# Kernel tuning notes

Measured on AMD Instinct MI355X. Metric: run time of the kernel, lower is better.

## Reference

```python
import jax, jax.numpy as jnp
import numpy as np

NUM_CAPSULE = 16
DIM_CAPSULE = 16
NUM_ROUTING = 3
EPS = 1e-7  # K.epsilon()


def squash(v, axis=-1):
    s2 = jnp.sum(jnp.square(v), axis=axis, keepdims=True) + EPS
    scale = s2 / ((1.0 + s2) * jnp.sqrt(s2))
    return scale * v


def setup_inputs() -> dict:
    key = jax.random.key(0)
    k1, k2 = jax.random.split(key)
    B, N, IC, ID = 64, 128, 32, 8
    x = jax.random.normal(k1, (B, N, IC, ID), dtype=jnp.float32)
    # glorot_uniform for W: [IC, ID, NUM_CAPSULE*DIM_CAPSULE]
    fan_in, fan_out = ID, NUM_CAPSULE * DIM_CAPSULE
    limit = np.sqrt(6.0 / (fan_in + fan_out))
    W = jax.random.uniform(k2, (IC, ID, NUM_CAPSULE * DIM_CAPSULE), dtype=jnp.float32,
                           minval=-limit, maxval=limit)
    return {"x": x, "W": W}


def reference(x, W):
    B, N, IC, ID = x.shape
    NC, DC = NUM_CAPSULE, DIM_CAPSULE
    u = x.reshape(-1, IC, ID)  # [BN, IC, ID]
    # prediction vectors: [BN, IC, NC*DC] -> [BN, NC, IC, DC]
    u_hat = jnp.einsum('bij,ijk->bik', u, W).reshape(-1, IC, NC, DC).transpose(0, 2, 1, 3)
    u_hat_stopped = jax.lax.stop_gradient(u_hat)
    b = jnp.zeros((u_hat.shape[0], NC, IC), dtype=x.dtype)
    outputs = None
    for i in range(NUM_ROUTING):
        c = jax.nn.softmax(b, axis=1)  # softmax over num_capsule axis (dim=1 in source)
        hat = u_hat if i == NUM_ROUTING - 1 else u_hat_stopped
        outputs = squash(jnp.einsum('bci,bcid->bcd', c, hat))  # [BN, NC, DC]
        if i < NUM_ROUTING - 1:
            b = b + jnp.einsum('bcd,bcid->bci', outputs, u_hat_stopped)
    return outputs.reshape(B, N, NC, DC)
```

## Files before the change

kernel.cpp:

```cpp
#include <hip/hip_runtime.h>
#include <hip/hip_bf16.h>


#define S 2

typedef float v2f __attribute__((ext_vector_type(2)));

__device__ __forceinline__ float bflo(unsigned u) { return __uint_as_float(u << 16); }
__device__ __forceinline__ float bfhi(unsigned u) { return __uint_as_float(u & 0xffff0000u); }

template <int CTRL>
__device__ __forceinline__ float dppf(float x) {
  return __builtin_bit_cast(float,
      __builtin_amdgcn_update_dpp(0, __builtin_bit_cast(int, x), CTRL, 0xF, 0xF, true));
}
template <int CTRL>
__device__ __forceinline__ v2f dpp2(v2f v) {
  v2f r;
  r.x = dppf<CTRL>(v.x);
  r.y = dppf<CTRL>(v.y);
  return r;
}
__device__ __forceinline__ float swz4(float x) {
  return __builtin_bit_cast(float,
      __builtin_amdgcn_ds_swizzle(__builtin_bit_cast(int, x), 0x101F));
}
__device__ __forceinline__ v2f swz4_2(v2f v) {
  v2f r;
  r.x = swz4(v.x);
  r.y = swz4(v.y);
  return r;
}

__global__ __launch_bounds__(256) void wt_kernel(const float* __restrict__ W,
                                                 unsigned short* __restrict__ Wt) {
  int o  = blockIdx.x * 256 + threadIdx.x;
  int ic = o >> 11;
  int k  = (o >> 3) & 255;
  int id = o & 7;
  Wt[o] = (unsigned short)(__bfloat16_as_ushort(__float2bfloat16(W[(ic * 8 + id) * 256 + k])));
}

__device__ __forceinline__ v2f squash2(v2f o) {
  v2f s2 = o * o;
  s2 += dpp2<0xB1>(s2);
  s2 += dpp2<0x4E>(s2);
  s2 += dpp2<0x141>(s2);
  s2 += dpp2<0x140>(s2);
  s2 += (v2f){1e-7f, 1e-7f};
  v2f sc;
  sc.x = s2.x * __builtin_amdgcn_rsqf(s2.x) * __builtin_amdgcn_rcpf(1.f + s2.x);
  sc.y = s2.y * __builtin_amdgcn_rsqf(s2.y) * __builtin_amdgcn_rcpf(1.f + s2.y);
  return o * sc;
}

template <bool ASSIGN>
__device__ __forceinline__ void b_update2(v2f v, const v2f* uh2, int dc,
                                          float* bp0, float* bp1) {
#pragma unroll
  for (int icb = 0; icb < 32; icb += 16) {
    v2f a[16];
#pragma unroll
    for (int j = 0; j < 16; ++j) a[j] = v * uh2[icb + j];
    v2f b8[8];
    const bool u8 = (dc & 8) != 0;
#pragma unroll
    for (int j = 0; j < 8; ++j) {
      v2f send = u8 ? a[j] : a[j + 8];
      v2f recv = dpp2<0x128>(send);
      b8[j] = (u8 ? a[j + 8] : a[j]) + recv;
    }
    v2f c4[4];
    const bool u4 = (dc & 4) != 0;
#pragma unroll
    for (int j = 0; j < 4; ++j) {
      v2f send = u4 ? b8[j] : b8[j + 4];
      v2f recv = swz4_2(send);
      c4[j] = (u4 ? b8[j + 4] : b8[j]) + recv;
    }
    v2f d2[2];
    const bool u2 = (dc & 2) != 0;
#pragma unroll
    for (int j = 0; j < 2; ++j) {
      v2f send = u2 ? c4[j] : c4[j + 2];
      v2f recv = dpp2<0x4E>(send);
      d2[j] = (u2 ? c4[j + 2] : c4[j]) + recv;
    }
    const bool u1 = (dc & 1) != 0;
    v2f send = u1 ? d2[0] : d2[1];
    v2f recv = dpp2<0xB1>(send);
    v2f e = (u1 ? d2[1] : d2[0]) + recv;
    if (ASSIGN) { bp0[icb + dc] = e.x;  bp1[icb + dc] = e.y; }
    else        { bp0[icb + dc] += e.x; bp1[icb + dc] += e.y; }
  }
}

__global__ __launch_bounds__(256, 3) void caps_kernel(const float* __restrict__ x,
                                                      const uint4* __restrict__ Wt4,
                                                      float* __restrict__ out) {
  const int t  = threadIdx.x;
  const int nc = t >> 4;
  const int dc = t & 15;
  const int s0 = blockIdx.x * S;

  __shared__ float b_lds[S][16][33];
  __shared__ __align__(16) float c_lds[16][72];

  v2f uh2[32];
  v2f o2 = (v2f){0.f, 0.f};

  const v2f* xu0 = (const v2f*)(x + (s0 + 0) * 256);
  const v2f* xu1 = (const v2f*)(x + (s0 + 1) * 256);
#pragma unroll
  for (int ic = 0; ic < 32; ++ic) {
    uint4 wv = Wt4[ic * 256 + t];
    v2f wp0 = (v2f){bflo(wv.x), bfhi(wv.x)};
    v2f wp1 = (v2f){bflo(wv.y), bfhi(wv.y)};
    v2f wp2 = (v2f){bflo(wv.z), bfhi(wv.z)};
    v2f wp3 = (v2f){bflo(wv.w), bfhi(wv.w)};
    v2f a0 = xu0[ic * 4 + 0] * wp0;
    a0 = __builtin_elementwise_fma(xu0[ic * 4 + 1], wp1, a0);
    a0 = __builtin_elementwise_fma(xu0[ic * 4 + 2], wp2, a0);
    a0 = __builtin_elementwise_fma(xu0[ic * 4 + 3], wp3, a0);
    v2f a1 = xu1[ic * 4 + 0] * wp0;
    a1 = __builtin_elementwise_fma(xu1[ic * 4 + 1], wp1, a1);
    a1 = __builtin_elementwise_fma(xu1[ic * 4 + 2], wp2, a1);
    a1 = __builtin_elementwise_fma(xu1[ic * 4 + 3], wp3, a1);
    v2f u = (v2f){a0.x + a0.y, a1.x + a1.y};
    uh2[ic] = u;
    o2 += u;
  }

  {
    v2f v = squash2(o2 * (v2f){0.0625f, 0.0625f});
    b_update2<true>(v, uh2, dc, &b_lds[0][nc][0], &b_lds[1][nc][0]);
  }
  __syncthreads();

#pragma unroll
  for (int r = 1; r < 3; ++r) {
    if (t < 64) {
      const int s = t >> 5, ic = t & 31;
      float e[16];
      float sum = 0.f;
#pragma unroll
      for (int n = 0; n < 16; ++n) { e[n] = __expf(b_lds[s][n][ic]); sum += e[n]; }
      const float inv = __builtin_amdgcn_rcpf(sum);
#pragma unroll
      for (int n = 0; n < 16; ++n) c_lds[n][2 * ic + s] = e[n] * inv;
    }
    __syncthreads();

    const float4* cp = (const float4*)&c_lds[nc][0];
    v2f o = (v2f){0.f, 0.f};
#pragma unroll
    for (int j = 0; j < 16; ++j) {
      float4 cc = cp[j];
      o = __builtin_elementwise_fma((v2f){cc.x, cc.y}, uh2[2 * j + 0], o);
      o = __builtin_elementwise_fma((v2f){cc.z, cc.w}, uh2[2 * j + 1], o);
    }
    v2f v = squash2(o);
    if (r == 2) {
      out[(s0 + 0) * 256 + t] = v.x;
      out[(s0 + 1) * 256 + t] = v.y;
    } else {
      b_update2<false>(v, uh2, dc, &b_lds[0][nc][0], &b_lds[1][nc][0]);
      __syncthreads();
    }
  }
}

extern "C" void kernel_launch(void* const* d_in, const int* in_sizes, int n_in,
                              void* d_out, int out_size, void* d_ws, size_t ws_size,
                              hipStream_t stream) {
  const float* x = (const float*)d_in[0];
  const float* W = (const float*)d_in[1];
  unsigned short* Wt = (unsigned short*)d_ws;

  wt_kernel<<<256, 256, 0, stream>>>(W, Wt);
  caps_kernel<<<8192 / S, 256, 0, stream>>>(x, (const uint4*)Wt, (float*)d_out);
}
```

Before: 107.0 us.

## Store transposed W as fp32 planes and software-prefetch next weight tile

The prepacked weight copy becomes fp32, laid out as two float4 planes per input capsule, so the main kernel loses its bf16 unpack shifts and masks. Each loop iteration loads the next input capsule's weights early as a software prefetch, and the occupancy hint goes from 3 to 4 blocks. The cost is twice the weight bytes read per block (L2-resident), more registers held for the prefetch while asking for higher occupancy, and precision now matching fp32 W rather than bf16.

```diff
diff --git a/kernel.cpp b/kernel.cpp
--- a/kernel.cpp
+++ b/kernel.cpp
@@ -5,9 +5,6 @@
 #define S 2
 
 typedef float v2f __attribute__((ext_vector_type(2)));
-
-__device__ __forceinline__ float bflo(unsigned u) { return __uint_as_float(u << 16); }
-__device__ __forceinline__ float bfhi(unsigned u) { return __uint_as_float(u & 0xffff0000u); }
 
 template <int CTRL>
 __device__ __forceinline__ float dppf(float x) {
@@ -33,12 +30,18 @@
 }
 
 __global__ __launch_bounds__(256) void wt_kernel(const float* __restrict__ W,
-                                                 unsigned short* __restrict__ Wt) {
-  int o  = blockIdx.x * 256 + threadIdx.x;
-  int ic = o >> 11;
-  int k  = (o >> 3) & 255;
-  int id = o & 7;
-  Wt[o] = (unsigned short)(__bfloat16_as_ushort(__float2bfloat16(W[(ic * 8 + id) * 256 + k])));
+                                                 float4* __restrict__ Wt) {
+  int o     = blockIdx.x * 256 + threadIdx.x;
+  int plane = o >> 13;
+  int ic    = (o >> 8) & 31;
+  int k     = o & 255;
+  const float* wp = &W[(ic * 8 + plane * 4) * 256 + k];
+  float4 v;
+  v.x = wp[0 * 256];
+  v.y = wp[1 * 256];
+  v.z = wp[2 * 256];
+  v.w = wp[3 * 256];
+  Wt[o] = v;
 }
 
 __device__ __forceinline__ v2f squash2(v2f o) {
@@ -95,8 +98,8 @@
   }
 }
 
-__global__ __launch_bounds__(256, 3) void caps_kernel(const float* __restrict__ x,
-                                                      const uint4* __restrict__ Wt4,
+__global__ __launch_bounds__(256, 4) void caps_kernel(const float* __restrict__ x,
+                                                      const float4* __restrict__ Wt4,
                                                       float* __restrict__ out) {
   const int t  = threadIdx.x;
   const int nc = t >> 4;
@@ -111,13 +114,17 @@
 
   const v2f* xu0 = (const v2f*)(x + (s0 + 0) * 256);
   const v2f* xu1 = (const v2f*)(x + (s0 + 1) * 256);
+  const float4* WA = Wt4;
+  const float4* WB = Wt4 + 8192;
+  float4 wa = WA[t], wb = WB[t];
 #pragma unroll
   for (int ic = 0; ic < 32; ++ic) {
-    uint4 wv = Wt4[ic * 256 + t];
-    v2f wp0 = (v2f){bflo(wv.x), bfhi(wv.x)};
-    v2f wp1 = (v2f){bflo(wv.y), bfhi(wv.y)};
-    v2f wp2 = (v2f){bflo(wv.z), bfhi(wv.z)};
-    v2f wp3 = (v2f){bflo(wv.w), bfhi(wv.w)};
+    float4 na, nb;
+    if (ic < 31) { na = WA[(ic + 1) * 256 + t]; nb = WB[(ic + 1) * 256 + t]; }
+    v2f wp0 = (v2f){wa.x, wa.y};
+    v2f wp1 = (v2f){wa.z, wa.w};
+    v2f wp2 = (v2f){wb.x, wb.y};
+    v2f wp3 = (v2f){wb.z, wb.w};
     v2f a0 = xu0[ic * 4 + 0] * wp0;
     a0 = __builtin_elementwise_fma(xu0[ic * 4 + 1], wp1, a0);
     a0 = __builtin_elementwise_fma(xu0[ic * 4 + 2], wp2, a0);
@@ -129,6 +136,8 @@
     v2f u = (v2f){a0.x + a0.y, a1.x + a1.y};
     uh2[ic] = u;
     o2 += u;
+    wa = na;
+    wb = nb;
   }
 
   {
@@ -175,8 +184,8 @@
                               hipStream_t stream) {
   const float* x = (const float*)d_in[0];
   const float* W = (const float*)d_in[1];
-  unsigned short* Wt = (unsigned short*)d_ws;
+  float4* Wt = (float4*)d_ws;
 
-  wt_kernel<<<256, 256, 0, stream>>>(W, Wt);
-  caps_kernel<<<8192 / S, 256, 0, stream>>>(x, (const uint4*)Wt, (float*)d_out);
+  wt_kernel<<<64, 256, 0, stream>>>(W, Wt);
+  caps_kernel<<<8192 / S, 256, 0, stream>>>(x, Wt, (float*)d_out);
 }
```

Result: slower. 109.4 us (+2.2%).

## Use fp16 dot2 for prediction vectors and parallelize routing softmax

Applied to the files above, without the earlier changes.

Converts W and x to fp16 in separate pre-kernels and computes the u_hat products with packed fp16 dot2 instructions instead of bf16 unpack plus fp32 FMAs. The routing softmax now runs on all 256 threads (four capsules per thread, combined with DPP reductions) instead of 64 threads. An extra __syncthreads is added after the last round. This adds a separate pass that reads all of x and writes it back as fp16, trading extra global traffic for fewer ALU ops and less input traffic in the main kernel. fp16 also introduces precision and range risk.

```diff
diff --git a/kernel.cpp b/kernel.cpp
--- a/kernel.cpp
+++ b/kernel.cpp
@@ -4,10 +4,8 @@
 
 #define S 2
 
-typedef float v2f __attribute__((ext_vector_type(2)));
-
-__device__ __forceinline__ float bflo(unsigned u) { return __uint_as_float(u << 16); }
-__device__ __forceinline__ float bfhi(unsigned u) { return __uint_as_float(u & 0xffff0000u); }
+typedef float    v2f __attribute__((ext_vector_type(2)));
+typedef _Float16 v2h __attribute__((ext_vector_type(2)));
 
 template <int CTRL>
 __device__ __forceinline__ float dppf(float x) {
@@ -32,13 +30,40 @@
   return r;
 }
 
+#if __has_builtin(__builtin_amdgcn_fdot2)
+__device__ __forceinline__ float dot2(v2h a, v2h b, float c) {
+  return __builtin_amdgcn_fdot2(a, b, c, false);
+}
+#else
+__device__ __forceinline__ float dot2(v2h a, v2h b, float c) {
+  return fmaf((float)a.x, (float)b.x, fmaf((float)a.y, (float)b.y, c));
+}
+#endif
+
 __global__ __launch_bounds__(256) void wt_kernel(const float* __restrict__ W,
-                                                 unsigned short* __restrict__ Wt) {
+                                                 _Float16* __restrict__ Wth) {
   int o  = blockIdx.x * 256 + threadIdx.x;
   int ic = o >> 11;
   int k  = (o >> 3) & 255;
   int id = o & 7;
-  Wt[o] = (unsigned short)(__bfloat16_as_ushort(__float2bfloat16(W[(ic * 8 + id) * 256 + k])));
+  Wth[o] = (_Float16)W[(ic * 8 + id) * 256 + k];
+}
+
+__global__ __launch_bounds__(256) void xh_kernel(const float* __restrict__ x,
+                                                 _Float16* __restrict__ xh) {
+  int tid = blockIdx.x * 256 + threadIdx.x;
+  const float4* xp = (const float4*)x + tid * 2;
+  float4 f0 = xp[0], f1 = xp[1];
+  v2h h0 = {(_Float16)f0.x, (_Float16)f0.y};
+  v2h h1 = {(_Float16)f0.z, (_Float16)f0.w};
+  v2h h2 = {(_Float16)f1.x, (_Float16)f1.y};
+  v2h h3 = {(_Float16)f1.z, (_Float16)f1.w};
+  uint4 o;
+  o.x = __builtin_bit_cast(unsigned, h0);
+  o.y = __builtin_bit_cast(unsigned, h1);
+  o.z = __builtin_bit_cast(unsigned, h2);
+  o.w = __builtin_bit_cast(unsigned, h3);
+  ((uint4*)xh)[tid] = o;
 }
 
 __device__ __forceinline__ v2f squash2(v2f o) {
@@ -95,7 +120,7 @@
   }
 }
 
-__global__ __launch_bounds__(256, 3) void caps_kernel(const float* __restrict__ x,
+__global__ __launch_bounds__(256, 3) void caps_kernel(const _Float16* __restrict__ xh,
                                                       const uint4* __restrict__ Wt4,
                                                       float* __restrict__ out) {
   const int t  = threadIdx.x;
@@ -104,29 +129,29 @@
   const int s0 = blockIdx.x * S;
 
   __shared__ float b_lds[S][16][33];
-  __shared__ __align__(16) float c_lds[16][72];
+  __shared__ __align__(16) float c_lds[16][68];
 
   v2f uh2[32];
   v2f o2 = (v2f){0.f, 0.f};
 
-  const v2f* xu0 = (const v2f*)(x + (s0 + 0) * 256);
-  const v2f* xu1 = (const v2f*)(x + (s0 + 1) * 256);
+  const v2h* xp0 = (const v2h*)(xh + (s0 + 0) * 256);
+  const v2h* xp1 = (const v2h*)(xh + (s0 + 1) * 256);
 #pragma unroll
   for (int ic = 0; ic < 32; ++ic) {
     uint4 wv = Wt4[ic * 256 + t];
-    v2f wp0 = (v2f){bflo(wv.x), bfhi(wv.x)};
-    v2f wp1 = (v2f){bflo(wv.y), bfhi(wv.y)};
-    v2f wp2 = (v2f){bflo(wv.z), bfhi(wv.z)};
-    v2f wp3 = (v2f){bflo(wv.w), bfhi(wv.w)};
-    v2f a0 = xu0[ic * 4 + 0] * wp0;
-    a0 = __builtin_elementwise_fma(xu0[ic * 4 + 1], wp1, a0);
-    a0 = __builtin_elementwise_fma(xu0[ic * 4 + 2], wp2, a0);
-    a0 = __builtin_elementwise_fma(xu0[ic * 4 + 3], wp3, a0);
-    v2f a1 = xu1[ic * 4 + 0] * wp0;
-    a1 = __builtin_elementwise_fma(xu1[ic * 4 + 1], wp1, a1);
-    a1 = __builtin_elementwise_fma(xu1[ic * 4 + 2], wp2, a1);
-    a1 = __builtin_elementwise_fma(xu1[ic * 4 + 3], wp3, a1);
-    v2f u = (v2f){a0.x + a0.y, a1.x + a1.y};
+    v2h w0 = __builtin_bit_cast(v2h, wv.x);
+    v2h w1 = __builtin_bit_cast(v2h, wv.y);
+    v2h w2 = __builtin_bit_cast(v2h, wv.z);
+    v2h w3 = __builtin_bit_cast(v2h, wv.w);
+    float a0 = dot2(xp0[ic * 4 + 3], w3,
+               dot2(xp0[ic * 4 + 2], w2,
+               dot2(xp0[ic * 4 + 1], w1,
+               dot2(xp0[ic * 4 + 0], w0, 0.f))));
+    float a1 = dot2(xp1[ic * 4 + 3], w3,
+               dot2(xp1[ic * 4 + 2], w2,
+               dot2(xp1[ic * 4 + 1], w1,
+               dot2(xp1[ic * 4 + 0], w0, 0.f))));
+    v2f u = (v2f){a0, a1};
     uh2[ic] = u;
     o2 += u;
   }
@@ -139,15 +164,22 @@
 
 #pragma unroll
   for (int r = 1; r < 3; ++r) {
-    if (t < 64) {
-      const int s = t >> 5, ic = t & 31;
-      float e[16];
-      float sum = 0.f;
-#pragma unroll
-      for (int n = 0; n < 16; ++n) { e[n] = __expf(b_lds[s][n][ic]); sum += e[n]; }
-      const float inv = __builtin_amdgcn_rcpf(sum);
-#pragma unroll
-      for (int n = 0; n < 16; ++n) c_lds[n][2 * ic + s] = e[n] * inv;
+    {
+      const int ss  = t >> 7;
+      const int icc = (t >> 2) & 31;
+      const int q   = t & 3;
+      float e0 = __expf(b_lds[ss][4 * q + 0][icc]);
+      float e1 = __expf(b_lds[ss][4 * q + 1][icc]);
+      float e2 = __expf(b_lds[ss][4 * q + 2][icc]);
+      float e3 = __expf(b_lds[ss][4 * q + 3][icc]);
+      float ps = (e0 + e1) + (e2 + e3);
+      ps += dppf<0xB1>(ps);
+      ps += dppf<0x4E>(ps);
+      float inv = __builtin_amdgcn_rcpf(ps);
+      c_lds[4 * q + 0][2 * icc + ss] = e0 * inv;
+      c_lds[4 * q + 1][2 * icc + ss] = e1 * inv;
+      c_lds[4 * q + 2][2 * icc + ss] = e2 * inv;
+      c_lds[4 * q + 3][2 * icc + ss] = e3 * inv;
     }
     __syncthreads();
 
@@ -165,8 +197,8 @@
       out[(s0 + 1) * 256 + t] = v.y;
     } else {
       b_update2<false>(v, uh2, dc, &b_lds[0][nc][0], &b_lds[1][nc][0]);
-      __syncthreads();
-    }
+    }
+    __syncthreads();
   }
 }
 
@@ -175,8 +207,10 @@
                               hipStream_t stream) {
   const float* x = (const float*)d_in[0];
   const float* W = (const float*)d_in[1];
-  unsigned short* Wt = (unsigned short*)d_ws;
-
-  wt_kernel<<<256, 256, 0, stream>>>(W, Wt);
-  caps_kernel<<<8192 / S, 256, 0, stream>>>(x, (const uint4*)Wt, (float*)d_out);
-}
+  _Float16* Wth = (_Float16*)d_ws;
+  _Float16* xh  = (_Float16*)d_ws + 65536;
+
+  wt_kernel<<<256, 256, 0, stream>>>(W, Wth);
+  xh_kernel<<<1024, 256, 0, stream>>>(x, xh);
+  caps_kernel<<<8192 / S, 256, 0, stream>>>(xh, (const uint4*)Wth, (float*)d_out);
+}
```

After: 98.95 us. -7.6%, faster.
